# Kernel optimization log

Hardware: AMD Instinct MI355X
Metric: run time of the kernel (lower is better)

## Reference

```python
import jax, jax.numpy as jnp
import numpy as np

MARGIN = 0.2
EPS = 1e-6  # torch.pairwise_distance default eps added to (x1 - x2)


def setup_inputs() -> dict:
    key = jax.random.key(0)
    k1, k2 = jax.random.split(key)
    N, D = 8192, 128
    x = jax.random.normal(k1, (N, D), dtype=jnp.float32)
    target = jax.random.randint(k2, (N,), 0, 1000)
    return {"x": x, "target": target}


def _pairwise_dist(x):
    # torch.pairwise_distance(x.unsqueeze(0), x.unsqueeze(1)):
    #   diff[i, j] = x[j] - x[i] + EPS ; dist[i, j] = ||diff[i, j]||_2
    # Expanded quadratic form avoids the [N, N, D] diff tensor:
    #   ||a - b + e||^2 = ||a||^2 + ||b||^2 - 2 a.b + 2e*sum(a - b) + D*e^2
    sq = jnp.sum(x * x, axis=1)          # [N]
    s = jnp.sum(x, axis=1)               # [N]
    dot = x @ x.T                        # [N, N]
    D = x.shape[1]
    d2 = (sq[None, :] + sq[:, None] - 2.0 * dot
          + 2.0 * EPS * (s[None, :] - s[:, None]) + D * EPS * EPS)
    return jnp.sqrt(jnp.maximum(d2, 0.0))


def reference(x, target):
    N = x.shape[0]
    dist = _pairwise_dist(x)                                 # [N, N]
    same = target[None, :] == target[:, None]                # [N, N] bool
    pos_mask = (same & ~jnp.eye(N, dtype=bool)).astype(x.dtype)
    hardest_pos = jnp.max(pos_mask * dist, axis=1, keepdims=True)  # [N, 1]
    neg_mask = (~same).astype(x.dtype)
    max_neg = jnp.max(dist, axis=1, keepdims=True)           # [N, 1]
    anchor_neg = dist + max_neg * (1.0 - neg_mask)           # push positives up
    hardest_neg = jnp.min(anchor_neg, axis=1, keepdims=True) # [N, 1]
    loss = jax.nn.relu(hardest_pos - hardest_neg + MARGIN)
    return jnp.mean(loss)
```

## Files before the change

kernel.cpp:

```cpp
#include <hip/hip_runtime.h>

#define N 8192
#define Dk 128
#define EPSC 1e-6f
#define MARGIN 0.2f

typedef __attribute__((ext_vector_type(8))) short bf16x8;
typedef __attribute__((ext_vector_type(4))) float f32x4;

__device__ __forceinline__ unsigned short f2bf(float f) {
    unsigned u = __float_as_uint(f);
    u = (u + 0x7FFFu + ((u >> 16) & 1u)) >> 16;
    return (unsigned short)u;
}
__device__ __forceinline__ unsigned enc(float f) {
    unsigned u = __float_as_uint(f);
    return (u & 0x80000000u) ? ~u : (u | 0x80000000u);
}
__device__ __forceinline__ float dec(unsigned u) {
    return __uint_as_float((u & 0x80000000u) ? (u & 0x7FFFFFFFu) : ~u);
}

__device__ __forceinline__ void gl_lds16(const void* src, void* lds_dst) {
    __builtin_amdgcn_global_load_lds(
        (const __attribute__((address_space(1))) unsigned*)src,
        (__attribute__((address_space(3))) unsigned*)lds_dst, 16, 0, 0);
}

__global__ void prep_kernel(const float* __restrict__ x, const int* __restrict__ tgt,
                            unsigned short* __restrict__ Xb, uint2* __restrict__ QT,
                            float* __restrict__ P,
                            unsigned* __restrict__ wsHp, unsigned* __restrict__ wsMn) {
    int row = blockIdx.x * 4 + (threadIdx.x >> 6);
    int l = threadIdx.x & 63;
    const float2 v = *reinterpret_cast<const float2*>(&x[row * Dk + l * 2]);
    float sq = fmaf(v.x, v.x, v.y * v.y);
    float s = v.x + v.y;
    ushort2 a;
    a.x = f2bf(v.x);
    a.y = f2bf(v.y);
    int c_phys = (l >> 2) ^ (row & 7);
    *reinterpret_cast<ushort2*>(&Xb[row * Dk + c_phys * 8 + 2 * (l & 3)]) = a;
#pragma unroll
    for (int m = 32; m >= 1; m >>= 1) {
        sq += __shfl_xor(sq, m);
        s += __shfl_xor(s, m);
    }
    if (l == 0) {
        P[row] = sq - 2.0f * EPSC * s;
        float Qj = sq + 2.0f * EPSC * s + (float)Dk * EPSC * EPSC;
        uint2 qt;
        qt.x = __float_as_uint(-0.5f * Qj);
        qt.y = (unsigned)tgt[row];
        QT[row] = qt;
        wsHp[row] = 0xFF800000u;
        wsMn[row] = 0x007FFFFFu;
    }
}

__global__ __launch_bounds__(256, 4) void main_kernel(
        const unsigned short* __restrict__ Xb,
        const uint2* __restrict__ QT, const int* __restrict__ tgt,
        unsigned* __restrict__ wsHp, unsigned* __restrict__ wsMn) {
    __shared__ unsigned short Bs[2][64 * Dk];
    __shared__ uint2 QTs[2][128];

    const int tid = threadIdx.x;
    const int w = tid >> 6;
    const int lane = tid & 63;
    const int n = lane & 15;
    const int q = lane >> 4;
    const int sw = n & 7;

    const int ig = (int)blockIdx.x >> 4;
    const int js = (int)blockIdx.x & 15;
    const int rbase = ig * 128 + 32 * w;

    const bf16x8* Xv = reinterpret_cast<const bf16x8*>(Xb);

    bf16x8 Af[2][4];
#pragma unroll
    for (int ti = 0; ti < 2; ++ti)
#pragma unroll
        for (int kk = 0; kk < 4; ++kk)
            Af[ti][kk] = Xv[(rbase + 16 * ti + n) * 16 + ((q + 4 * kk) ^ sw)];

    int tsl[8];
#pragma unroll
    for (int ti = 0; ti < 2; ++ti) {
        int4 t4 = *reinterpret_cast<const int4*>(&tgt[rbase + 16 * ti + 4 * q]);
        tsl[4 * ti + 0] = t4.x;
        tsl[4 * ti + 1] = t4.y;
        tsl[4 * ti + 2] = t4.z;
        tsl[4 * ti + 3] = t4.w;
    }

    float hp[8], mn[8];
#pragma unroll
    for (int s = 0; s < 8; ++s) {
        hp[s] = INFINITY;
        mn[s] = -INFINITY;
    }

    auto stage = [&](int step) {
        const int jb = js * 512 + step * 64;
        const int buf = step & 1;
#pragma unroll
        for (int t = 0; t < 4; ++t)
            gl_lds16(&Xb[(jb + 16 * w + 4 * t) * Dk] + lane * 8,
                     &Bs[buf][(16 * w + 4 * t) * Dk]);
        if (w == 0)
            gl_lds16(reinterpret_cast<const unsigned short*>(&QT[jb]) + lane * 8,
                     &QTs[buf][0]);
    };

    stage(0);

    for (int step = 0; step < 8; ++step) {
        const int buf = step & 1;
        if (step < 7) {
            stage(step + 1);
            if (w == 0)
                asm volatile("s_waitcnt vmcnt(5)" ::: "memory");
            else
                asm volatile("s_waitcnt vmcnt(4)" ::: "memory");
        } else {
            asm volatile("s_waitcnt vmcnt(0)" ::: "memory");
        }
        __builtin_amdgcn_sched_barrier(0);
        __builtin_amdgcn_s_barrier();
        __builtin_amdgcn_sched_barrier(0);

        float Qv[4];
        int tv[4];
#pragma unroll
        for (int tj = 0; tj < 4; ++tj) {
            uint2 qt = QTs[buf][16 * tj + n];
            Qv[tj] = __uint_as_float(qt.x);
            tv[tj] = (int)qt.y;
        }

        f32x4 acc[2][4];
#pragma unroll
        for (int ti = 0; ti < 2; ++ti)
#pragma unroll
            for (int tj = 0; tj < 4; ++tj) acc[ti][tj] = Qv[tj];

#pragma unroll
        for (int kk = 0; kk < 4; ++kk) {
            bf16x8 Bf[4];
#pragma unroll
            for (int tj = 0; tj < 4; ++tj)
                Bf[tj] = *reinterpret_cast<const bf16x8*>(
                    &Bs[buf][(16 * tj + n) * Dk + (((q + 4 * kk) ^ sw) << 3)]);
            __builtin_amdgcn_s_setprio(1);
#pragma unroll
            for (int ti = 0; ti < 2; ++ti)
#pragma unroll
                for (int tj = 0; tj < 4; ++tj)
                    acc[ti][tj] = __builtin_amdgcn_mfma_f32_16x16x32_bf16(Af[ti][kk], Bf[tj],
                                                                          acc[ti][tj], 0, 0, 0);
            __builtin_amdgcn_s_setprio(0);
        }

#pragma unroll
        for (int tj = 0; tj < 4; ++tj) {
            int tvv = tv[tj];
#pragma unroll
            for (int ti = 0; ti < 2; ++ti) {
                f32x4 v = acc[ti][tj];
                int e0 = tvv == tsl[4 * ti + 0];
                int e1 = tvv == tsl[4 * ti + 1];
                int e2 = tvv == tsl[4 * ti + 2];
                int e3 = tvv == tsl[4 * ti + 3];
                if (__ballot(e0 | e1 | e2 | e3)) {
                    hp[4 * ti + 0] = fminf(hp[4 * ti + 0], e0 ? v[0] : INFINITY);
                    hp[4 * ti + 1] = fminf(hp[4 * ti + 1], e1 ? v[1] : INFINITY);
                    hp[4 * ti + 2] = fminf(hp[4 * ti + 2], e2 ? v[2] : INFINITY);
                    hp[4 * ti + 3] = fminf(hp[4 * ti + 3], e3 ? v[3] : INFINITY);
                    mn[4 * ti + 0] = fmaxf(mn[4 * ti + 0], e0 ? -INFINITY : v[0]);
                    mn[4 * ti + 1] = fmaxf(mn[4 * ti + 1], e1 ? -INFINITY : v[1]);
                    mn[4 * ti + 2] = fmaxf(mn[4 * ti + 2], e2 ? -INFINITY : v[2]);
                    mn[4 * ti + 3] = fmaxf(mn[4 * ti + 3], e3 ? -INFINITY : v[3]);
                } else {
                    mn[4 * ti + 0] = fmaxf(mn[4 * ti + 0], v[0]);
                    mn[4 * ti + 1] = fmaxf(mn[4 * ti + 1], v[1]);
                    mn[4 * ti + 2] = fmaxf(mn[4 * ti + 2], v[2]);
                    mn[4 * ti + 3] = fmaxf(mn[4 * ti + 3], v[3]);
                }
            }
        }
    }

#pragma unroll
    for (int m = 1; m <= 8; m <<= 1) {
#pragma unroll
        for (int s = 0; s < 8; ++s) {
            hp[s] = fminf(hp[s], __shfl_xor(hp[s], m));
            mn[s] = fmaxf(mn[s], __shfl_xor(mn[s], m));
        }
    }
    if (n == 0) {
#pragma unroll
        for (int ti = 0; ti < 2; ++ti) {
#pragma unroll
            for (int r = 0; r < 4; ++r) {
                int i = rbase + 16 * ti + 4 * q + r;
                atomicMin(&wsHp[i], enc(hp[4 * ti + r]));
                atomicMax(&wsMn[i], enc(mn[4 * ti + r]));
            }
        }
    }
}

__global__ void finish_kernel(const float* __restrict__ P,
                              const unsigned* __restrict__ wsHp,
                              const unsigned* __restrict__ wsMn,
                              float* __restrict__ out) {
    int t = threadIdx.x;
    float sum = 0.0f;
#pragma unroll
    for (int h = 0; h < 2; ++h) {
        int base = 8 * t + 4 * h;
        float4 Pv = *reinterpret_cast<const float4*>(&P[base]);
        uint4 Hv = *reinterpret_cast<const uint4*>(&wsHp[base]);
        uint4 Mv = *reinterpret_cast<const uint4*>(&wsMn[base]);
        const float* Pf = &Pv.x;
        const unsigned* Hu = &Hv.x;
        const unsigned* Mu = &Mv.x;
#pragma unroll
        for (int k = 0; k < 4; ++k) {
            float hp = sqrtf(fmaxf(fmaf(-2.0f, dec(Hu[k]), Pf[k]), 0.0f));
            float hn = sqrtf(fmaxf(fmaf(-2.0f, dec(Mu[k]), Pf[k]), 0.0f));
            sum += fmaxf(hp - hn + MARGIN, 0.0f);
        }
    }
#pragma unroll
    for (int m = 32; m >= 1; m >>= 1) sum += __shfl_xor(sum, m);
    __shared__ float ws[16];
    if ((t & 63) == 0) ws[t >> 6] = sum;
    __syncthreads();
    if (t == 0) {
        float tot = 0.0f;
#pragma unroll
        for (int i = 0; i < 16; ++i) tot += ws[i];
        out[0] = tot * (1.0f / (float)N);
    }
}

extern "C" void kernel_launch(void* const* d_in, const int* in_sizes, int n_in,
                              void* d_out, int out_size, void* d_ws, size_t ws_size,
                              hipStream_t stream) {
    const float* x = (const float*)d_in[0];
    const int* tgt = (const int*)d_in[1];
    float* out = (float*)d_out;

    char* ws = (char*)d_ws;
    const size_t xb = (size_t)N * Dk * 2;
    unsigned short* Xb = (unsigned short*)ws;
    uint2* QT = (uint2*)(ws + xb);
    float* P = (float*)(ws + xb + (size_t)N * 8);
    unsigned* wsHp = (unsigned*)(ws + xb + (size_t)N * 12);
    unsigned* wsMn = (unsigned*)(ws + xb + (size_t)N * 16);

    prep_kernel<<<N / 4, 256, 0, stream>>>(x, tgt, Xb, QT, P, wsHp, wsMn);
    main_kernel<<<1024, 256, 0, stream>>>(Xb, QT, tgt, wsHp, wsMn);
    finish_kernel<<<1, 1024, 0, stream>>>(P, wsHp, wsMn, out);
}
```

Measured before the change: 98.21 us.

## Sort rows by class so positive masks become contiguous index ranges

Adds a histogram, a prefix scan and a counting-sort scatter in the prep step, so rows are permuted into class-contiguous order. Each row then carries a packed [start,end) range of its class. The main kernel can test per tile whether any positives are possible and take a max-only path otherwise, which replaces per-element label compares and ballots. The cost is two extra kernel launches plus a memset and atomics during prep, and row order now depends on atomic scheduling.

```diff
diff --git a/kernel.cpp b/kernel.cpp
--- a/kernel.cpp
+++ b/kernel.cpp
@@ -4,6 +4,7 @@
 #define Dk 128
 #define EPSC 1e-6f
 #define MARGIN 0.2f
+#define NCLS 1000
 
 typedef __attribute__((ext_vector_type(8))) short bf16x8;
 typedef __attribute__((ext_vector_type(4))) float f32x4;
@@ -27,9 +28,36 @@
         (__attribute__((address_space(3))) unsigned*)lds_dst, 16, 0, 0);
 }
 
+__global__ void hist_kernel(const int* __restrict__ tgt, int* __restrict__ cnt) {
+    int i = blockIdx.x * 1024 + threadIdx.x;
+    if (i < N) atomicAdd(&cnt[tgt[i]], 1);
+}
+
+__global__ void scan_kernel(const int* __restrict__ cnt, int* __restrict__ cursor,
+                            int* __restrict__ SEclass) {
+    __shared__ int sbuf[1024];
+    int t = threadIdx.x;
+    int v = (t < NCLS) ? cnt[t] : 0;
+    sbuf[t] = v;
+    __syncthreads();
+#pragma unroll
+    for (int off = 1; off < 1024; off <<= 1) {
+        int add = (t >= off) ? sbuf[t - off] : 0;
+        __syncthreads();
+        sbuf[t] += add;
+        __syncthreads();
+    }
+    if (t < NCLS) {
+        int base = sbuf[t] - v;
+        cursor[t] = base;
+        SEclass[t] = base | ((base + v) << 16);
+    }
+}
+
 __global__ void prep_kernel(const float* __restrict__ x, const int* __restrict__ tgt,
-                            unsigned short* __restrict__ Xb, uint2* __restrict__ QT,
-                            float* __restrict__ P,
+                            int* __restrict__ cursor, const int* __restrict__ SEclass,
+                            unsigned short* __restrict__ Xb, float* __restrict__ Qf,
+                            float* __restrict__ P, int* __restrict__ SE,
                             unsigned* __restrict__ wsHp, unsigned* __restrict__ wsMn) {
     int row = blockIdx.x * 4 + (threadIdx.x >> 6);
     int l = threadIdx.x & 63;
@@ -39,31 +67,37 @@
     ushort2 a;
     a.x = f2bf(v.x);
     a.y = f2bf(v.y);
-    int c_phys = (l >> 2) ^ (row & 7);
-    *reinterpret_cast<ushort2*>(&Xb[row * Dk + c_phys * 8 + 2 * (l & 3)]) = a;
+    int dest = 0, se = 0;
+    if (l == 0) {
+        int c = tgt[row];
+        dest = atomicAdd(&cursor[c], 1);
+        se = SEclass[c];
+    }
+    dest = __shfl(dest, 0);
+    se = __shfl(se, 0);
+    int c_phys = (l >> 2) ^ (dest & 7);
+    *reinterpret_cast<ushort2*>(&Xb[dest * Dk + c_phys * 8 + 2 * (l & 3)]) = a;
 #pragma unroll
     for (int m = 32; m >= 1; m >>= 1) {
         sq += __shfl_xor(sq, m);
         s += __shfl_xor(s, m);
     }
     if (l == 0) {
-        P[row] = sq - 2.0f * EPSC * s;
+        P[dest] = sq - 2.0f * EPSC * s;
         float Qj = sq + 2.0f * EPSC * s + (float)Dk * EPSC * EPSC;
-        uint2 qt;
-        qt.x = __float_as_uint(-0.5f * Qj);
-        qt.y = (unsigned)tgt[row];
-        QT[row] = qt;
-        wsHp[row] = 0xFF800000u;
-        wsMn[row] = 0x007FFFFFu;
+        Qf[dest] = -0.5f * Qj;
+        SE[dest] = se;
+        wsHp[dest] = 0xFF800000u;
+        wsMn[dest] = 0x007FFFFFu;
     }
 }
 
 __global__ __launch_bounds__(256, 4) void main_kernel(
-        const unsigned short* __restrict__ Xb,
-        const uint2* __restrict__ QT, const int* __restrict__ tgt,
+        const unsigned short* __restrict__ Xb, const float* __restrict__ Qf,
+        const int* __restrict__ SE,
         unsigned* __restrict__ wsHp, unsigned* __restrict__ wsMn) {
     __shared__ unsigned short Bs[2][64 * Dk];
-    __shared__ uint2 QTs[2][128];
+    __shared__ float Qs[2][256];
 
     const int tid = threadIdx.x;
     const int w = tid >> 6;
@@ -85,15 +119,17 @@
         for (int kk = 0; kk < 4; ++kk)
             Af[ti][kk] = Xv[(rbase + 16 * ti + n) * 16 + ((q + 4 * kk) ^ sw)];
 
-    int tsl[8];
+    unsigned sePack[8];
 #pragma unroll
     for (int ti = 0; ti < 2; ++ti) {
-        int4 t4 = *reinterpret_cast<const int4*>(&tgt[rbase + 16 * ti + 4 * q]);
-        tsl[4 * ti + 0] = t4.x;
-        tsl[4 * ti + 1] = t4.y;
-        tsl[4 * ti + 2] = t4.z;
-        tsl[4 * ti + 3] = t4.w;
-    }
+        int4 s4 = *reinterpret_cast<const int4*>(&SE[rbase + 16 * ti + 4 * q]);
+        sePack[4 * ti + 0] = (unsigned)s4.x;
+        sePack[4 * ti + 1] = (unsigned)s4.y;
+        sePack[4 * ti + 2] = (unsigned)s4.z;
+        sePack[4 * ti + 3] = (unsigned)s4.w;
+    }
+    const int uS = SE[rbase] & 0xffff;
+    const int uE = ((unsigned)SE[rbase + 31]) >> 16;
 
     float hp[8], mn[8];
 #pragma unroll
@@ -110,14 +146,15 @@
             gl_lds16(&Xb[(jb + 16 * w + 4 * t) * Dk] + lane * 8,
                      &Bs[buf][(16 * w + 4 * t) * Dk]);
         if (w == 0)
-            gl_lds16(reinterpret_cast<const unsigned short*>(&QT[jb]) + lane * 8,
-                     &QTs[buf][0]);
+            gl_lds16(reinterpret_cast<const char*>(&Qf[jb]) + lane * 16,
+                     &Qs[buf][0]);
     };
 
     stage(0);
 
     for (int step = 0; step < 8; ++step) {
         const int buf = step & 1;
+        const int jb = js * 512 + step * 64;
         if (step < 7) {
             stage(step + 1);
             if (w == 0)
@@ -132,13 +169,8 @@
         __builtin_amdgcn_sched_barrier(0);
 
         float Qv[4];
-        int tv[4];
-#pragma unroll
-        for (int tj = 0; tj < 4; ++tj) {
-            uint2 qt = QTs[buf][16 * tj + n];
-            Qv[tj] = __uint_as_float(qt.x);
-            tv[tj] = (int)qt.y;
-        }
+#pragma unroll
+        for (int tj = 0; tj < 4; ++tj) Qv[tj] = Qs[buf][16 * tj + n];
 
         f32x4 acc[2][4];
 #pragma unroll
@@ -163,32 +195,33 @@
             __builtin_amdgcn_s_setprio(0);
         }
 
-#pragma unroll
-        for (int tj = 0; tj < 4; ++tj) {
-            int tvv = tv[tj];
-#pragma unroll
-            for (int ti = 0; ti < 2; ++ti) {
-                f32x4 v = acc[ti][tj];
-                int e0 = tvv == tsl[4 * ti + 0];
-                int e1 = tvv == tsl[4 * ti + 1];
-                int e2 = tvv == tsl[4 * ti + 2];
-                int e3 = tvv == tsl[4 * ti + 3];
-                if (__ballot(e0 | e1 | e2 | e3)) {
-                    hp[4 * ti + 0] = fminf(hp[4 * ti + 0], e0 ? v[0] : INFINITY);
-                    hp[4 * ti + 1] = fminf(hp[4 * ti + 1], e1 ? v[1] : INFINITY);
-                    hp[4 * ti + 2] = fminf(hp[4 * ti + 2], e2 ? v[2] : INFINITY);
-                    hp[4 * ti + 3] = fminf(hp[4 * ti + 3], e3 ? v[3] : INFINITY);
-                    mn[4 * ti + 0] = fmaxf(mn[4 * ti + 0], e0 ? -INFINITY : v[0]);
-                    mn[4 * ti + 1] = fmaxf(mn[4 * ti + 1], e1 ? -INFINITY : v[1]);
-                    mn[4 * ti + 2] = fmaxf(mn[4 * ti + 2], e2 ? -INFINITY : v[2]);
-                    mn[4 * ti + 3] = fmaxf(mn[4 * ti + 3], e3 ? -INFINITY : v[3]);
-                } else {
+        if ((jb < uE) && (uS < jb + 64)) {
+#pragma unroll
+            for (int tj = 0; tj < 4; ++tj) {
+                int j = jb + 16 * tj + n;
+#pragma unroll
+                for (int ti = 0; ti < 2; ++ti) {
+                    f32x4 v = acc[ti][tj];
+#pragma unroll
+                    for (int r = 0; r < 4; ++r) {
+                        unsigned se = sePack[4 * ti + r];
+                        int inb = (j >= (int)(se & 0xffffu)) && (j < (int)(se >> 16));
+                        hp[4 * ti + r] = fminf(hp[4 * ti + r], inb ? v[r] : INFINITY);
+                        mn[4 * ti + r] = fmaxf(mn[4 * ti + r], inb ? -INFINITY : v[r]);
+                    }
+                }
+            }
+        } else {
+#pragma unroll
+            for (int tj = 0; tj < 4; ++tj)
+#pragma unroll
+                for (int ti = 0; ti < 2; ++ti) {
+                    f32x4 v = acc[ti][tj];
                     mn[4 * ti + 0] = fmaxf(mn[4 * ti + 0], v[0]);
                     mn[4 * ti + 1] = fmaxf(mn[4 * ti + 1], v[1]);
                     mn[4 * ti + 2] = fmaxf(mn[4 * ti + 2], v[2]);
                     mn[4 * ti + 3] = fmaxf(mn[4 * ti + 3], v[3]);
                 }
-            }
         }
     }
 
@@ -258,12 +291,20 @@
     char* ws = (char*)d_ws;
     const size_t xb = (size_t)N * Dk * 2;
     unsigned short* Xb = (unsigned short*)ws;
-    uint2* QT = (uint2*)(ws + xb);
-    float* P = (float*)(ws + xb + (size_t)N * 8);
-    unsigned* wsHp = (unsigned*)(ws + xb + (size_t)N * 12);
-    unsigned* wsMn = (unsigned*)(ws + xb + (size_t)N * 16);
-
-    prep_kernel<<<N / 4, 256, 0, stream>>>(x, tgt, Xb, QT, P, wsHp, wsMn);
-    main_kernel<<<1024, 256, 0, stream>>>(Xb, QT, tgt, wsHp, wsMn);
+    float* Qf = (float*)(ws + xb);
+    float* P = (float*)(ws + xb + (size_t)N * 4);
+    unsigned* wsHp = (unsigned*)(ws + xb + (size_t)N * 8);
+    unsigned* wsMn = (unsigned*)(ws + xb + (size_t)N * 12);
+    int* SE = (int*)(ws + xb + (size_t)N * 16);
+    int* cursor = (int*)(ws + xb + (size_t)N * 20);
+    int* SEclass = (int*)(ws + xb + (size_t)N * 20 + 4096);
+    int* cnt = (int*)(ws + xb + (size_t)N * 20 + 8192);
+
+    hipMemsetAsync(cnt, 0, 4096, stream);
+    hist_kernel<<<N / 1024, 1024, 0, stream>>>(tgt, cnt);
+    scan_kernel<<<1, 1024, 0, stream>>>(cnt, cursor, SEclass);
+    prep_kernel<<<N / 4, 256, 0, stream>>>(x, tgt, cursor, SEclass, Xb, Qf, P, SE,
+                                           wsHp, wsMn);
+    main_kernel<<<1024, 256, 0, stream>>>(Xb, Qf, SE, wsHp, wsMn);
     finish_kernel<<<1, 1024, 0, stream>>>(P, wsHp, wsMn, out);
 }
```

Result: slower. 103.3 us (+5.1%).
